# Performance work log

Measured on AMD Instinct MI355X. Metric: run time of the kernel, lower is better.

Reference implementation:

```python
import jax, jax.numpy as jnp
import numpy as np
from jax import lax


def _bayer_kernels():
    # 5 fixed 3x3 interpolation stencils (identity, plus-avg, cross-avg, h-avg, v-avg)
    k5 = np.array([
        [[0, 0, 0], [0, 1, 0], [0, 0, 0]],
        [[0, .25, 0], [.25, 0, .25], [0, .25, 0]],
        [[.25, 0, .25], [0, 0, 0], [.25, 0, .25]],
        [[0, 0, 0], [.5, 0, .5], [0, 0, 0]],
        [[0, .5, 0], [0, 0, 0], [0, .5, 0]],
    ], dtype=np.float32)  # (5,3,3)
    # 4 fixed (3,5) selection matrices (1x1 convs per Bayer quadrant)
    sel = np.array([
        [[0, 0, 1, 0, 0], [0, 1, 0, 0, 0], [1, 0, 0, 0, 0]],
        [[0, 0, 0, 0, 1], [1, 0, 0, 0, 0], [0, 0, 0, 1, 0]],
        [[0, 0, 0, 1, 0], [1, 0, 0, 0, 0], [0, 0, 0, 0, 1]],
        [[1, 0, 0, 0, 0], [0, 1, 0, 0, 0], [0, 0, 1, 0, 0]],
    ], dtype=np.float32)  # (4,3,5)
    return jnp.asarray(k5), jnp.asarray(sel)


def setup_inputs() -> dict:
    key = jax.random.key(0)
    x = jax.random.uniform(key, (2, 1, 4096, 4096), dtype=jnp.float32) * 255.0
    k5, sel = _bayer_kernels()
    return {"x": x, "kernels5": k5, "sel": sel}


def reference(x, kernels5, sel):
    n, _, h, w = x.shape
    x_pad = jnp.pad(x, ((0, 0), (0, 0), (1, 1), (1, 1)), mode="reflect")
    # 3x3 stencil bank: (N,1,H+2,W+2) -> (N,5,H,W)
    xc = lax.conv_general_dilated(
        x_pad, kernels5.reshape(5, 1, 3, 3), window_strides=(1, 1),
        padding="VALID", dimension_numbers=("NCHW", "OIHW", "NCHW"))
    h2, w2 = h // 2, w // 2
    # pixel-unshuffle (DCR order): (N,5,H,W) -> (N, 2,2, 5, H/2, W/2) -> (N,4,5,H/2,W/2)
    u = xc.reshape(n, 5, h2, 2, w2, 2).transpose(0, 3, 5, 1, 2, 4).reshape(n, 4, 5, h2, w2)
    # per-quadrant 1x1 selection conv: (N,4,3,H/2,W/2)
    e = jnp.einsum("qos,nqsxy->nqoxy", sel, u)
    # pixel-shuffle (DCR order): (N,4,3,H/2,W/2) -> (N,3,H,W)
    y = e.reshape(n, 2, 2, 3, h2, w2).transpose(0, 3, 4, 1, 5, 2).reshape(n, 3, h, w)
    return y
```

## Files before the change

kernel.cpp:

```cpp
#include <hip/hip_runtime.h>


#define IMG_H 4096
#define IMG_W 4096

__global__ __launch_bounds__(256) void bayer_demosaic_kernel(
    const float* __restrict__ x, float* __restrict__ out) {
    const int jg = blockIdx.x * blockDim.x + threadIdx.x;
    const int i  = blockIdx.y;
    const int n  = blockIdx.z;
    const int j  = jg << 2;

    const float* xn = x + (size_t)n * IMG_H * IMG_W;

    const int im = (i == 0) ? 1 : i - 1;
    const int ip = (i == IMG_H - 1) ? IMG_H - 2 : i + 1;

    const float* rowm = xn + (size_t)im * IMG_W;
    const float* rowc = xn + (size_t)i  * IMG_W;
    const float* rowp = xn + (size_t)ip * IMG_W;

    float a[6], b[6], c[6];
    {
        const float4 va = *(const float4*)(rowm + j);
        const float4 vb = *(const float4*)(rowc + j);
        const float4 vc = *(const float4*)(rowp + j);
        a[1] = va.x; a[2] = va.y; a[3] = va.z; a[4] = va.w;
        b[1] = vb.x; b[2] = vb.y; b[3] = vb.z; b[4] = vb.w;
        c[1] = vc.x; c[2] = vc.y; c[3] = vc.z; c[4] = vc.w;
        if (j == 0) { a[0] = va.y; b[0] = vb.y; c[0] = vc.y; }
        else        { a[0] = rowm[j - 1]; b[0] = rowc[j - 1]; c[0] = rowp[j - 1]; }
        if (j == IMG_W - 4) { a[5] = va.z; b[5] = vb.z; c[5] = vc.z; }
        else        { a[5] = rowm[j + 4]; b[5] = rowc[j + 4]; c[5] = rowp[j + 4]; }
    }

    float o0[4], o1[4], o2[4];
    const int dy = i & 1;
#pragma unroll
    for (int k = 0; k < 4; ++k) {
        const float center = b[k + 1];
        const float plus   = 0.25f * (a[k + 1] + c[k + 1] + b[k] + b[k + 2]);
        const float cross  = 0.25f * (a[k] + a[k + 2] + c[k] + c[k + 2]);
        const float havg   = 0.5f  * (b[k] + b[k + 2]);
        const float vavg   = 0.5f  * (a[k + 1] + c[k + 1]);
        if (dy == 0) {
            if ((k & 1) == 0) { o0[k] = cross; o1[k] = plus;   o2[k] = center; }
            else              { o0[k] = vavg;  o1[k] = center; o2[k] = havg;   }
        } else {
            if ((k & 1) == 0) { o0[k] = havg;  o1[k] = center; o2[k] = vavg;   }
            else              { o0[k] = center; o1[k] = plus;  o2[k] = cross;  }
        }
    }

    float* on = out + (size_t)n * 3 * IMG_H * IMG_W;
    const size_t off = (size_t)i * IMG_W + j;
    const size_t plane = (size_t)IMG_H * IMG_W;
    *(float4*)(on + off)             = make_float4(o0[0], o0[1], o0[2], o0[3]);
    *(float4*)(on + plane + off)     = make_float4(o1[0], o1[1], o1[2], o1[3]);
    *(float4*)(on + 2 * plane + off) = make_float4(o2[0], o2[1], o2[2], o2[3]);
}

extern "C" void kernel_launch(void* const* d_in, const int* in_sizes, int n_in,
                              void* d_out, int out_size, void* d_ws, size_t ws_size,
                              hipStream_t stream) {
    const float* x = (const float*)d_in[0];
    float* out = (float*)d_out;

    const int N = 2;
    dim3 block(256, 1, 1);
    dim3 grid(IMG_W / 4 / 256, IMG_H, N);
    bayer_demosaic_kernel<<<grid, block, 0, stream>>>(x, out);
}
```

Before: 530.5 us.

## Process two rows per thread, share halo via wave shuffles, use nontemporal stores

Each thread now computes a pair of Bayer rows (even and odd) from four loaded input rows, so the two middle rows are reused instead of being reloaded by separate threads, and the grid height is halved. Left and right halo pixels come from neighbouring lanes via __shfl_up/__shfl_down, with scalar loads kept only for the wavefront edge lanes. The output is written with nontemporal stores to avoid polluting cache with write-only data. Risks include a higher register count, and the shuffles assume 64-wide wavefronts with contiguous lanes.

```diff
diff --git a/kernel.cpp b/kernel.cpp
--- a/kernel.cpp
+++ b/kernel.cpp
@@ -4,60 +4,85 @@
 #define IMG_H 4096
 #define IMG_W 4096
 
+typedef float v4f __attribute__((ext_vector_type(4)));
+
+__device__ __forceinline__ void load_win(const float* __restrict__ rowp, int j,
+                                         int lane, float w[6]) {
+    const float4 v = *(const float4*)(rowp + j);
+    w[1] = v.x; w[2] = v.y; w[3] = v.z; w[4] = v.w;
+    float left  = __shfl_up(v.w, 1);
+    float right = __shfl_down(v.x, 1);
+    if (lane == 0)  left  = (j == 0) ? v.y : rowp[j - 1];
+    if (lane == 63) right = (j == IMG_W - 4) ? v.z : rowp[j + 4];
+    w[0] = left; w[5] = right;
+}
+
 __global__ __launch_bounds__(256) void bayer_demosaic_kernel(
     const float* __restrict__ x, float* __restrict__ out) {
-    const int jg = blockIdx.x * blockDim.x + threadIdx.x;
-    const int i  = blockIdx.y;
-    const int n  = blockIdx.z;
-    const int j  = jg << 2;
+    const int jg   = blockIdx.x * blockDim.x + threadIdx.x;
+    const int r    = blockIdx.y << 1;
+    const int n    = blockIdx.z;
+    const int j    = jg << 2;
+    const int lane = threadIdx.x & 63;
 
     const float* xn = x + (size_t)n * IMG_H * IMG_W;
 
-    const int im = (i == 0) ? 1 : i - 1;
-    const int ip = (i == IMG_H - 1) ? IMG_H - 2 : i + 1;
+    const int rm = (r == 0) ? 1 : r - 1;
+    const int rp = (r == IMG_H - 2) ? IMG_H - 2 : r + 2;
 
-    const float* rowm = xn + (size_t)im * IMG_W;
-    const float* rowc = xn + (size_t)i  * IMG_W;
-    const float* rowp = xn + (size_t)ip * IMG_W;
+    const float* rowA = xn + (size_t)rm * IMG_W;
+    const float* rowB = xn + (size_t)r  * IMG_W;
+    const float* rowC = xn + (size_t)(r + 1) * IMG_W;
+    const float* rowD = xn + (size_t)rp * IMG_W;
 
-    float a[6], b[6], c[6];
-    {
-        const float4 va = *(const float4*)(rowm + j);
-        const float4 vb = *(const float4*)(rowc + j);
-        const float4 vc = *(const float4*)(rowp + j);
-        a[1] = va.x; a[2] = va.y; a[3] = va.z; a[4] = va.w;
-        b[1] = vb.x; b[2] = vb.y; b[3] = vb.z; b[4] = vb.w;
-        c[1] = vc.x; c[2] = vc.y; c[3] = vc.z; c[4] = vc.w;
-        if (j == 0) { a[0] = va.y; b[0] = vb.y; c[0] = vc.y; }
-        else        { a[0] = rowm[j - 1]; b[0] = rowc[j - 1]; c[0] = rowp[j - 1]; }
-        if (j == IMG_W - 4) { a[5] = va.z; b[5] = vb.z; c[5] = vc.z; }
-        else        { a[5] = rowm[j + 4]; b[5] = rowc[j + 4]; c[5] = rowp[j + 4]; }
-    }
+    float a[6], b[6], c[6], d[6];
+    load_win(rowA, j, lane, a);
+    load_win(rowB, j, lane, b);
+    load_win(rowC, j, lane, c);
+    load_win(rowD, j, lane, d);
 
-    float o0[4], o1[4], o2[4];
-    const int dy = i & 1;
+    float e0[4], e1[4], e2[4];
+    float f0[4], f1[4], f2[4];
 #pragma unroll
     for (int k = 0; k < 4; ++k) {
-        const float center = b[k + 1];
-        const float plus   = 0.25f * (a[k + 1] + c[k + 1] + b[k] + b[k + 2]);
-        const float cross  = 0.25f * (a[k] + a[k + 2] + c[k] + c[k + 2]);
-        const float havg   = 0.5f  * (b[k] + b[k + 2]);
-        const float vavg   = 0.5f  * (a[k + 1] + c[k + 1]);
-        if (dy == 0) {
-            if ((k & 1) == 0) { o0[k] = cross; o1[k] = plus;   o2[k] = center; }
-            else              { o0[k] = vavg;  o1[k] = center; o2[k] = havg;   }
-        } else {
-            if ((k & 1) == 0) { o0[k] = havg;  o1[k] = center; o2[k] = vavg;   }
-            else              { o0[k] = center; o1[k] = plus;  o2[k] = cross;  }
+        {
+            const float center = b[k + 1];
+            const float plus   = 0.25f * (a[k + 1] + c[k + 1] + b[k] + b[k + 2]);
+            const float cross  = 0.25f * (a[k] + a[k + 2] + c[k] + c[k + 2]);
+            const float havg   = 0.5f  * (b[k] + b[k + 2]);
+            const float vavg   = 0.5f  * (a[k + 1] + c[k + 1]);
+            if ((k & 1) == 0) { e0[k] = cross; e1[k] = plus;   e2[k] = center; }
+            else              { e0[k] = vavg;  e1[k] = center; e2[k] = havg;   }
+        }
+        {
+            const float center = c[k + 1];
+            const float plus   = 0.25f * (b[k + 1] + d[k + 1] + c[k] + c[k + 2]);
+            const float cross  = 0.25f * (b[k] + b[k + 2] + d[k] + d[k + 2]);
+            const float havg   = 0.5f  * (c[k] + c[k + 2]);
+            const float vavg   = 0.5f  * (b[k + 1] + d[k + 1]);
+            if ((k & 1) == 0) { f0[k] = havg;   f1[k] = center; f2[k] = vavg;  }
+            else              { f0[k] = center; f1[k] = plus;   f2[k] = cross; }
         }
     }
 
     float* on = out + (size_t)n * 3 * IMG_H * IMG_W;
-    const size_t off = (size_t)i * IMG_W + j;
     const size_t plane = (size_t)IMG_H * IMG_W;
-    *(float4*)(on + off)             = make_float4(o0[0], o0[1], o0[2], o0[3]);
-    *(float4*)(on + plane + off)     = make_float4(o1[0], o1[1], o1[2], o1[3]);
-    *(float4*)(on + 2 * plane + off) = make_float4(o2[0], o2[1], o2[2], o2[3]);
+    const size_t off0  = (size_t)r * IMG_W + j;
+    const size_t off1  = off0 + IMG_W;
+
+    v4f t;
+    t = (v4f){e0[0], e0[1], e0[2], e0[3]};
+    __builtin_nontemporal_store(t, (v4f*)(on + off0));
+    t = (v4f){f0[0], f0[1], f0[2], f0[3]};
+    __builtin_nontemporal_store(t, (v4f*)(on + off1));
+    t = (v4f){e1[0], e1[1], e1[2], e1[3]};
+    __builtin_nontemporal_store(t, (v4f*)(on + plane + off0));
+    t = (v4f){f1[0], f1[1], f1[2], f1[3]};
+    __builtin_nontemporal_store(t, (v4f*)(on + plane + off1));
+    t = (v4f){e2[0], e2[1], e2[2], e2[3]};
+    __builtin_nontemporal_store(t, (v4f*)(on + 2 * plane + off0));
+    t = (v4f){f2[0], f2[1], f2[2], f2[3]};
+    __builtin_nontemporal_store(t, (v4f*)(on + 2 * plane + off1));
 }
 
 extern "C" void kernel_launch(void* const* d_in, const int* in_sizes, int n_in,
@@ -68,6 +93,6 @@
 
     const int N = 2;
     dim3 block(256, 1, 1);
-    dim3 grid(IMG_W / 4 / 256, IMG_H, N);
+    dim3 grid(IMG_W / 4 / 256, IMG_H / 2, N);
     bayer_demosaic_kernel<<<grid, block, 0, stream>>>(x, out);
 }
```

New measurement: 488.6 us. 7.9% less time.

## Process two rows and two column chunks per thread with shuffled halos and nontemporal stores

Applied to the files above, without the earlier changes.

Each thread now computes a 2x8 output tile (two Bayer rows, two float4 chunks 256 columns apart), loading four input rows instead of three per output row, which cuts redundant row reads. Halo neighbor pixels come from wavefront shuffles instead of extra scalar global loads, and outputs are written with nontemporal stores to avoid polluting cache. It also removes the row-parity branch because each thread knows its even/odd row. The cost is higher register use per thread and a grid with a quarter of the threads.

```diff
diff --git a/kernel.cpp b/kernel.cpp
--- a/kernel.cpp
+++ b/kernel.cpp
@@ -4,60 +4,105 @@
 #define IMG_H 4096
 #define IMG_W 4096
 
+typedef float v4f __attribute__((ext_vector_type(4)));
+
+#define NTST(p, a0, a1, a2, a3)                                   \
+    {                                                             \
+        v4f s_ = (v4f){a0, a1, a2, a3};                           \
+        __builtin_nontemporal_store(s_, (v4f*)(p));               \
+    }
+
+__device__ __forceinline__ void load_win2(const float* __restrict__ rowp,
+                                          int j0, int j1, int lane,
+                                          float w0[6], float w1[6]) {
+    const float4 vA = *(const float4*)(rowp + j0);
+    const float4 vB = *(const float4*)(rowp + j1);
+    w0[1] = vA.x; w0[2] = vA.y; w0[3] = vA.z; w0[4] = vA.w;
+    w1[1] = vB.x; w1[2] = vB.y; w1[3] = vB.z; w1[4] = vB.w;
+    float lA = __shfl_up(vA.w, 1);
+    float rA = __shfl_down(vA.x, 1);
+    float lB = __shfl_up(vB.w, 1);
+    float rB = __shfl_down(vB.x, 1);
+    const float brA = __shfl(vB.x, 0);
+    const float blB = __shfl(vA.w, 63);
+    if (lane == 63) rA = brA;
+    if (lane == 0)  lB = blB;
+    if (lane == 0)  lA = (j0 == 0) ? vA.y : rowp[j0 - 1];
+    if (lane == 63) rB = (j1 == IMG_W - 4) ? vB.z : rowp[j1 + 4];
+    w0[0] = lA; w0[5] = rA;
+    w1[0] = lB; w1[5] = rB;
+}
+
+struct Out6 { float e0[4], e1[4], e2[4], f0[4], f1[4], f2[4]; };
+
+__device__ __forceinline__ void compute_pair(const float a[6], const float b[6],
+                                             const float c[6], const float d[6],
+                                             Out6& o) {
+#pragma unroll
+    for (int k = 0; k < 4; ++k) {
+        {
+            const float center = b[k + 1];
+            const float plus   = 0.25f * (a[k + 1] + c[k + 1] + b[k] + b[k + 2]);
+            const float cross  = 0.25f * (a[k] + a[k + 2] + c[k] + c[k + 2]);
+            const float havg   = 0.5f  * (b[k] + b[k + 2]);
+            const float vavg   = 0.5f  * (a[k + 1] + c[k + 1]);
+            if ((k & 1) == 0) { o.e0[k] = cross; o.e1[k] = plus;   o.e2[k] = center; }
+            else              { o.e0[k] = vavg;  o.e1[k] = center; o.e2[k] = havg;   }
+        }
+        {
+            const float center = c[k + 1];
+            const float plus   = 0.25f * (b[k + 1] + d[k + 1] + c[k] + c[k + 2]);
+            const float cross  = 0.25f * (b[k] + b[k + 2] + d[k] + d[k + 2]);
+            const float havg   = 0.5f  * (c[k] + c[k + 2]);
+            const float vavg   = 0.5f  * (b[k + 1] + d[k + 1]);
+            if ((k & 1) == 0) { o.f0[k] = havg;   o.f1[k] = center; o.f2[k] = vavg;  }
+            else              { o.f0[k] = center; o.f1[k] = plus;   o.f2[k] = cross; }
+        }
+    }
+}
+
 __global__ __launch_bounds__(256) void bayer_demosaic_kernel(
     const float* __restrict__ x, float* __restrict__ out) {
-    const int jg = blockIdx.x * blockDim.x + threadIdx.x;
-    const int i  = blockIdx.y;
-    const int n  = blockIdx.z;
-    const int j  = jg << 2;
+    const int lane  = threadIdx.x & 63;
+    const int wv    = threadIdx.x >> 6;
+    const int wbase = blockIdx.x * 2048 + wv * 512;
+    const int j0    = wbase + (lane << 2);
+    const int j1    = j0 + 256;
+    const int n     = blockIdx.z;
+    const int r     = blockIdx.y << 1;
 
     const float* xn = x + (size_t)n * IMG_H * IMG_W;
+    float* on       = out + (size_t)n * 3 * IMG_H * IMG_W;
+    const size_t plane = (size_t)IMG_H * IMG_W;
 
-    const int im = (i == 0) ? 1 : i - 1;
-    const int ip = (i == IMG_H - 1) ? IMG_H - 2 : i + 1;
+    const int rm = (r == 0) ? 1 : r - 1;
+    const int rp = (r == IMG_H - 2) ? IMG_H - 2 : r + 2;
 
-    const float* rowm = xn + (size_t)im * IMG_W;
-    const float* rowc = xn + (size_t)i  * IMG_W;
-    const float* rowp = xn + (size_t)ip * IMG_W;
+    float a0[6], a1[6], b0[6], b1[6], c0[6], c1[6], d0[6], d1[6];
+    load_win2(xn + (size_t)rm * IMG_W,      j0, j1, lane, a0, a1);
+    load_win2(xn + (size_t)r  * IMG_W,      j0, j1, lane, b0, b1);
+    load_win2(xn + (size_t)(r + 1) * IMG_W, j0, j1, lane, c0, c1);
+    load_win2(xn + (size_t)rp * IMG_W,      j0, j1, lane, d0, d1);
 
-    float a[6], b[6], c[6];
-    {
-        const float4 va = *(const float4*)(rowm + j);
-        const float4 vb = *(const float4*)(rowc + j);
-        const float4 vc = *(const float4*)(rowp + j);
-        a[1] = va.x; a[2] = va.y; a[3] = va.z; a[4] = va.w;
-        b[1] = vb.x; b[2] = vb.y; b[3] = vb.z; b[4] = vb.w;
-        c[1] = vc.x; c[2] = vc.y; c[3] = vc.z; c[4] = vc.w;
-        if (j == 0) { a[0] = va.y; b[0] = vb.y; c[0] = vc.y; }
-        else        { a[0] = rowm[j - 1]; b[0] = rowc[j - 1]; c[0] = rowp[j - 1]; }
-        if (j == IMG_W - 4) { a[5] = va.z; b[5] = vb.z; c[5] = vc.z; }
-        else        { a[5] = rowm[j + 4]; b[5] = rowc[j + 4]; c[5] = rowp[j + 4]; }
-    }
+    Out6 oA, oB;
+    compute_pair(a0, b0, c0, d0, oA);
+    compute_pair(a1, b1, c1, d1, oB);
 
-    float o0[4], o1[4], o2[4];
-    const int dy = i & 1;
-#pragma unroll
-    for (int k = 0; k < 4; ++k) {
-        const float center = b[k + 1];
-        const float plus   = 0.25f * (a[k + 1] + c[k + 1] + b[k] + b[k + 2]);
-        const float cross  = 0.25f * (a[k] + a[k + 2] + c[k] + c[k + 2]);
-        const float havg   = 0.5f  * (b[k] + b[k + 2]);
-        const float vavg   = 0.5f  * (a[k + 1] + c[k + 1]);
-        if (dy == 0) {
-            if ((k & 1) == 0) { o0[k] = cross; o1[k] = plus;   o2[k] = center; }
-            else              { o0[k] = vavg;  o1[k] = center; o2[k] = havg;   }
-        } else {
-            if ((k & 1) == 0) { o0[k] = havg;  o1[k] = center; o2[k] = vavg;   }
-            else              { o0[k] = center; o1[k] = plus;  o2[k] = cross;  }
-        }
-    }
+    const size_t off0 = (size_t)r * IMG_W + j0;
+    const size_t off1 = off0 + IMG_W;
 
-    float* on = out + (size_t)n * 3 * IMG_H * IMG_W;
-    const size_t off = (size_t)i * IMG_W + j;
-    const size_t plane = (size_t)IMG_H * IMG_W;
-    *(float4*)(on + off)             = make_float4(o0[0], o0[1], o0[2], o0[3]);
-    *(float4*)(on + plane + off)     = make_float4(o1[0], o1[1], o1[2], o1[3]);
-    *(float4*)(on + 2 * plane + off) = make_float4(o2[0], o2[1], o2[2], o2[3]);
+    NTST(on + off0,                 oA.e0[0], oA.e0[1], oA.e0[2], oA.e0[3]);
+    NTST(on + off0 + 256,           oB.e0[0], oB.e0[1], oB.e0[2], oB.e0[3]);
+    NTST(on + off1,                 oA.f0[0], oA.f0[1], oA.f0[2], oA.f0[3]);
+    NTST(on + off1 + 256,           oB.f0[0], oB.f0[1], oB.f0[2], oB.f0[3]);
+    NTST(on + plane + off0,         oA.e1[0], oA.e1[1], oA.e1[2], oA.e1[3]);
+    NTST(on + plane + off0 + 256,   oB.e1[0], oB.e1[1], oB.e1[2], oB.e1[3]);
+    NTST(on + plane + off1,         oA.f1[0], oA.f1[1], oA.f1[2], oA.f1[3]);
+    NTST(on + plane + off1 + 256,   oB.f1[0], oB.f1[1], oB.f1[2], oB.f1[3]);
+    NTST(on + 2 * plane + off0,     oA.e2[0], oA.e2[1], oA.e2[2], oA.e2[3]);
+    NTST(on + 2 * plane + off0 + 256, oB.e2[0], oB.e2[1], oB.e2[2], oB.e2[3]);
+    NTST(on + 2 * plane + off1,     oA.f2[0], oA.f2[1], oA.f2[2], oA.f2[3]);
+    NTST(on + 2 * plane + off1 + 256, oB.f2[0], oB.f2[1], oB.f2[2], oB.f2[3]);
 }
 
 extern "C" void kernel_launch(void* const* d_in, const int* in_sizes, int n_in,
@@ -68,6 +113,6 @@
 
     const int N = 2;
     dim3 block(256, 1, 1);
-    dim3 grid(IMG_W / 4 / 256, IMG_H, N);
+    dim3 grid(IMG_W / 2048, IMG_H / 2, N);
     bayer_demosaic_kernel<<<grid, block, 0, stream>>>(x, out);
 }
```

Result: faster. 486.7 us (-8.3%).
